# Kernel optimization log

Hardware: AMD Instinct MI355X
Metric: run time of the kernel (lower is better)

## Reference

```python
import jax, jax.numpy as jnp
import numpy as np

# Key observation: the TF module groups ROIs per image (boolean_mask), runs the
# same MLP on each group, concatenates the ragged results, then argsort-gathers
# to restore the ORIGINAL row order. Since the Dense/ReLU MLP acts row-wise and
# identically for every image, the group -> MLP -> regroup pipeline is exactly
# equivalent to applying the MLP to all rows in their original order. The clean
# JAX reference therefore computes the same math with a single fused GEMM chain.

NUM_CLASSES = 81
HIDDEN_DIM = 1024
N = 2048          # total ROIs
SS = 7            # sample_size
FS = 256          # feature_size
FEAT_DIM = SS * SS * FS  # 12544
NUM_IMAGES = 8


def setup_inputs() -> dict:
    key = jax.random.key(0)
    ks = jax.random.split(key, 8)
    features = jax.random.normal(ks[0], (N, SS, SS, FS), dtype=jnp.float32)
    batch_indices = jnp.sort(jax.random.randint(ks[1], (N,), 0, NUM_IMAGES, dtype=jnp.int32))
    s1 = 1.0 / np.sqrt(FEAT_DIM)
    s2 = 1.0 / np.sqrt(HIDDEN_DIM)
    W1 = jax.random.uniform(ks[2], (FEAT_DIM, HIDDEN_DIM), jnp.float32, -s1, s1)
    b1 = jnp.zeros((HIDDEN_DIM,), jnp.float32)
    W2 = jax.random.uniform(ks[3], (HIDDEN_DIM, HIDDEN_DIM), jnp.float32, -s2, s2)
    b2 = jnp.zeros((HIDDEN_DIM,), jnp.float32)
    Wc = jax.random.uniform(ks[4], (HIDDEN_DIM, NUM_CLASSES), jnp.float32, -s2, s2)
    bc = jnp.zeros((NUM_CLASSES,), jnp.float32)
    return {"features": features, "batch_indices": batch_indices,
            "W1": W1, "b1": b1, "W2": W2, "b2": b2, "Wc": Wc, "bc": bc}


def reference(features, batch_indices, W1, b1, W2, b2, Wc, bc):
    # Group/ungroup in the original is an identity permutation on rows, but we
    # reproduce it explicitly and cheaply: stable-sort rows by image id, run the
    # MLP, then invert the permutation via argsort (same as TF argsort-gather).
    order = jnp.argsort(batch_indices, stable=True)          # group rows per image
    x = features[order].reshape(features.shape[0], -1)       # [N, feat_dim]
    x = jax.nn.relu(x @ W1 + b1)
    x = jax.nn.relu(x @ W2 + b2)
    logits = x @ Wc + bc                                     # [N, num_classes]
    inv = jnp.argsort(order)                                 # restore original order
    return logits[inv]
```

## Files before the change

kernel.cpp:

```cpp
#include <hip/hip_runtime.h>
#include <hip/hip_bf16.h>
#include <stdint.h>

typedef __bf16 bf16_t;
typedef __bf16 bf16x2 __attribute__((ext_vector_type(2)));
typedef __bf16 bf16x4 __attribute__((ext_vector_type(4)));
typedef __bf16 bf16x8 __attribute__((ext_vector_type(8)));
typedef float f32x4 __attribute__((ext_vector_type(4)));

__device__ __forceinline__ void async_ld16(const bf16_t* g, bf16_t* lds) {
    __builtin_amdgcn_global_load_lds(
        (__attribute__((address_space(1))) void*)g,
        (__attribute__((address_space(3))) void*)lds,
        16, 0, 0);
}

__device__ __forceinline__ void wait_vm0() {
    asm volatile("s_waitcnt vmcnt(0)" ::: "memory");
}


__device__ __forceinline__ void transpose_tile(
    const float* __restrict__ in, bf16_t* __restrict__ out,
    int R, int C, int Cp, int tileIdx, int tid, float (*tile)[33])
{
    const int tilesX = Cp / 32;
    const int c0 = (tileIdx % tilesX) * 32;
    const int r0 = (tileIdx / tilesX) * 32;
    const int tx = tid & 31;
    const int ty = tid >> 5;
#pragma unroll
    for (int i = 0; i < 32; i += 8) {
        int rr = r0 + ty + i, cc = c0 + tx;
        float v = 0.f;
        if (cc < C) v = in[(size_t)rr * C + cc];
        tile[ty + i][tx] = v;
    }
    __syncthreads();
    const int px = tid & 15;
    const int py = tid >> 4;
#pragma unroll
    for (int i = 0; i < 32; i += 16) {
        int oc = c0 + py + i;
        int orr = r0 + px * 2;
        bf16x2 o = { (bf16_t)tile[px * 2][py + i], (bf16_t)tile[px * 2 + 1][py + i] };
        *(bf16x2*)&out[(size_t)oc * R + orr] = o;
    }
}

__global__ void prep_all(const float* __restrict__ X, bf16_t* __restrict__ Xb, int n4,
                         const float* __restrict__ W1, bf16_t* __restrict__ W1T,
                         const float* __restrict__ W2, bf16_t* __restrict__ W2T,
                         const float* __restrict__ Wc, bf16_t* __restrict__ WcT,
                         int FEAT, int HID, int NC, int NCP,
                         int nCvt, int t1, int t2)
{
    __shared__ float tile[32][33];
    int bid = blockIdx.x;
    int tid = threadIdx.x;
    if (bid < nCvt) {
        int i = bid * 256 + tid;
        if (i < n4) {
            float4 v = ((const float4*)X)[i];
            bf16x4 o = { (bf16_t)v.x, (bf16_t)v.y, (bf16_t)v.z, (bf16_t)v.w };
            ((bf16x4*)Xb)[i] = o;
        }
        return;
    }
    bid -= nCvt;
    if (bid < t1) { transpose_tile(W1, W1T, FEAT, HID, HID, bid, tid, tile); return; }
    bid -= t1;
    if (bid < t2) { transpose_tile(W2, W2T, HID, HID, HID, bid, tid, tile); return; }
    bid -= t2;
    transpose_tile(Wc, WcT, HID, NC, NCP, bid, tid, tile);
}

__global__ __launch_bounds__(256, 2) void gemm128_bk64(
    const bf16_t* __restrict__ A, const bf16_t* __restrict__ B,
    float* __restrict__ P, int M, int N, int K, int KC)
{
    __shared__ __align__(16) bf16_t Asm[2][128 * 64];
    __shared__ __align__(16) bf16_t Bsm[2][128 * 64];

    const int tid  = threadIdx.x;
    const int wave = tid >> 6;
    const int lane = tid & 63;
    const int bm = blockIdx.x, bn = blockIdx.y, s = blockIdx.z;

    const int Koff = s * KC;
    const int Kc   = (K - Koff < KC) ? (K - Koff) : KC;
    const int nt   = Kc >> 6;

    const bf16_t* Ab = A + (size_t)bm * 128 * K + Koff;
    const bf16_t* Bb = B + (size_t)bn * 128 * K + Koff;

    const int sr = lane >> 3;
    const int sk = ((lane & 7) ^ (sr & 7)) * 8;

    const int wm = (wave >> 1) * 64;
    const int wn = (wave & 1) * 64;
    const int r  = lane & 15;
    const int q  = lane >> 4;

    f32x4 acc[4][4];
#pragma unroll
    for (int i = 0; i < 4; ++i)
#pragma unroll
        for (int j = 0; j < 4; ++j)
            acc[i][j] = f32x4{0.f, 0.f, 0.f, 0.f};

    auto issue = [&](int t, int buf) {
#pragma unroll
        for (int i = 0; i < 4; ++i) {
            const int rb = wave * 32 + i * 8;
            async_ld16(Ab + (size_t)(rb + sr) * K + (t * 64 + sk), &Asm[buf][rb * 64]);
            async_ld16(Bb + (size_t)(rb + sr) * K + (t * 64 + sk), &Bsm[buf][rb * 64]);
        }
    };

    issue(0, 0);
    wait_vm0();
    __builtin_amdgcn_s_barrier();

    int cur = 0;
    for (int t = 0; t < nt; ++t) {
        const bool more = (t + 1 < nt);
        if (more) issue(t + 1, cur ^ 1);

#pragma unroll
        for (int rnd = 0; rnd < 2; ++rnd) {
            bf16x8 af[4], bfr[4];
#pragma unroll
            for (int i = 0; i < 4; ++i)
                af[i] = *(const bf16x8*)&Asm[cur][(wm + i * 16 + r) * 64
                                                  + ((rnd * 4 + q) ^ (r & 7)) * 8];
#pragma unroll
            for (int j = 0; j < 4; ++j)
                bfr[j] = *(const bf16x8*)&Bsm[cur][(wn + j * 16 + r) * 64
                                                   + ((rnd * 4 + q) ^ (r & 7)) * 8];
#pragma unroll
            for (int i = 0; i < 4; ++i)
#pragma unroll
                for (int j = 0; j < 4; ++j)
                    acc[i][j] = __builtin_amdgcn_mfma_f32_16x16x32_bf16(af[i], bfr[j], acc[i][j], 0, 0, 0);
        }

        if (more) {
            wait_vm0();
            __builtin_amdgcn_s_barrier();
            cur ^= 1;
        }
    }

    float* Pb = P + ((size_t)s * M + (size_t)bm * 128) * N + (size_t)bn * 128;
    const int r4 = q * 4;
#pragma unroll
    for (int i = 0; i < 4; ++i)
#pragma unroll
        for (int j = 0; j < 4; ++j)
#pragma unroll
            for (int rg = 0; rg < 4; ++rg)
                Pb[(size_t)(wm + i * 16 + r4 + rg) * N + (wn + j * 16 + r)] = acc[i][j][rg];
}

template <bool RELU, typename OutT>
__global__ __launch_bounds__(256, 4) void gemm64_fused(
    const bf16_t* __restrict__ A, const bf16_t* __restrict__ B,
    const float* __restrict__ bias, OutT* __restrict__ out,
    int K, int Nout)
{
    __shared__ __align__(16) bf16_t Asm[2][64 * 64];
    __shared__ __align__(16) bf16_t Bsm[2][64 * 64];

    const int tid  = threadIdx.x;
    const int wave = tid >> 6;
    const int lane = tid & 63;
    const int bm = blockIdx.x, bn = blockIdx.y;

    const bf16_t* Ab = A + (size_t)bm * 64 * K;
    const bf16_t* Bb = B + (size_t)bn * 64 * K;

    const int sr = lane >> 3;
    const int sk = ((lane & 7) ^ (sr & 7)) * 8;

    const int wm = (wave >> 1) * 32;
    const int wn = (wave & 1) * 32;
    const int r  = lane & 15;
    const int q  = lane >> 4;
    const int nt = K >> 6;

    f32x4 acc[2][2];
#pragma unroll
    for (int i = 0; i < 2; ++i)
#pragma unroll
        for (int j = 0; j < 2; ++j)
            acc[i][j] = f32x4{0.f, 0.f, 0.f, 0.f};

    auto issue = [&](int t, int buf) {
#pragma unroll
        for (int i = 0; i < 2; ++i) {
            const int rb = wave * 16 + i * 8;
            async_ld16(Ab + (size_t)(rb + sr) * K + (t * 64 + sk), &Asm[buf][rb * 64]);
            async_ld16(Bb + (size_t)(rb + sr) * K + (t * 64 + sk), &Bsm[buf][rb * 64]);
        }
    };

    issue(0, 0);
    wait_vm0();
    __builtin_amdgcn_s_barrier();

    int cur = 0;
    for (int t = 0; t < nt; ++t) {
        const bool more = (t + 1 < nt);
        if (more) issue(t + 1, cur ^ 1);

#pragma unroll
        for (int rnd = 0; rnd < 2; ++rnd) {
            bf16x8 af[2], bfr[2];
#pragma unroll
            for (int i = 0; i < 2; ++i)
                af[i] = *(const bf16x8*)&Asm[cur][(wm + i * 16 + r) * 64
                                                  + ((rnd * 4 + q) ^ (r & 7)) * 8];
#pragma unroll
            for (int j = 0; j < 2; ++j)
                bfr[j] = *(const bf16x8*)&Bsm[cur][(wn + j * 16 + r) * 64
                                                   + ((rnd * 4 + q) ^ (r & 7)) * 8];
#pragma unroll
            for (int i = 0; i < 2; ++i)
#pragma unroll
                for (int j = 0; j < 2; ++j)
                    acc[i][j] = __builtin_amdgcn_mfma_f32_16x16x32_bf16(af[i], bfr[j], acc[i][j], 0, 0, 0);
        }

        if (more) {
            wait_vm0();
            __builtin_amdgcn_s_barrier();
            cur ^= 1;
        }
    }

    const int r4 = (lane >> 4) * 4;
    const int c  = lane & 15;
#pragma unroll
    for (int i = 0; i < 2; ++i)
#pragma unroll
        for (int j = 0; j < 2; ++j) {
            const int col = bn * 64 + wn + j * 16 + c;
            if (col < Nout) {
                const float bv = bias[col];
#pragma unroll
                for (int rg = 0; rg < 4; ++rg) {
                    const int row = bm * 64 + wm + i * 16 + r4 + rg;
                    float v = acc[i][j][rg] + bv;
                    if (RELU) v = fmaxf(v, 0.f);
                    out[(size_t)row * Nout + col] = (OutT)v;
                }
            }
        }
}


template <int S>
__global__ void reduce_relu_bf16_k(const float* __restrict__ P, const float* __restrict__ bias,
                                   bf16_t* __restrict__ h, int MN, int Nm1) {
    int i4 = (blockIdx.x * 256 + threadIdx.x) * 4;
    if (i4 >= MN) return;
    int n = i4 & Nm1;
    float4 a = *(const float4*)(bias + n);
#pragma unroll
    for (int s = 0; s < S; ++s) {
        float4 p = *(const float4*)(P + (size_t)s * MN + i4);
        a.x += p.x; a.y += p.y; a.z += p.z; a.w += p.w;
    }
    a.x = fmaxf(a.x, 0.f); a.y = fmaxf(a.y, 0.f);
    a.z = fmaxf(a.z, 0.f); a.w = fmaxf(a.w, 0.f);
    bf16x4 o = { (bf16_t)a.x, (bf16_t)a.y, (bf16_t)a.z, (bf16_t)a.w };
    *(bf16x4*)(h + i4) = o;
}


extern "C" void kernel_launch(void* const* d_in, const int* in_sizes, int n_in,
                              void* d_out, int out_size, void* d_ws, size_t ws_size,
                              hipStream_t stream) {
    const float* X  = (const float*)d_in[0];
    const float* W1 = (const float*)d_in[2];
    const float* b1 = (const float*)d_in[3];
    const float* W2 = (const float*)d_in[4];
    const float* b2 = (const float*)d_in[5];
    const float* Wc = (const float*)d_in[6];
    const float* bc = (const float*)d_in[7];
    float* out = (float*)d_out;

    const int M    = in_sizes[1];
    const int FEAT = in_sizes[0] / M;
    const int HID  = in_sizes[3];
    const int NC   = in_sizes[7];
    const int NCP  = 128;

    char* ws = (char*)d_ws;
    size_t off = 0;
    auto alloc = [&](size_t bytes) {
        char* p = ws + off;
        off += (bytes + 255) & ~(size_t)255;
        return p;
    };
    bf16_t* Xb  = (bf16_t*)alloc((size_t)M * FEAT * 2);
    bf16_t* W1T = (bf16_t*)alloc((size_t)FEAT * HID * 2);
    bf16_t* W2T = (bf16_t*)alloc((size_t)HID * HID * 2);
    bf16_t* WcT = (bf16_t*)alloc((size_t)NCP * HID * 2);
    bf16_t* h1  = (bf16_t*)alloc((size_t)M * HID * 2);
    bf16_t* h2  = (bf16_t*)alloc((size_t)M * HID * 2);
    float*  P   = (float*)(ws + off);

    size_t rem  = ws_size > off ? ws_size - off : 0;
    size_t perS = (size_t)M * HID * 4;
    int S1 = (rem >= 4 * perS) ? 4 : (rem >= 2 * perS) ? 2 : 1;
    int KC1 = ((FEAT / S1 + 63) / 64) * 64;

    int n4   = (M * FEAT) / 4;
    int nCvt = (n4 + 255) / 256;
    int t1 = (HID / 32) * (FEAT / 32);
    int t2 = (HID / 32) * (HID / 32);
    int t3 = (NCP / 32) * (HID / 32);
    prep_all<<<nCvt + t1 + t2 + t3, 256, 0, stream>>>(
        X, Xb, n4, W1, W1T, W2, W2T, Wc, WcT, FEAT, HID, NC, NCP, nCvt, t1, t2);

    gemm128_bk64<<<dim3(M / 128, HID / 128, S1), 256, 0, stream>>>(Xb, W1T, P, M, HID, FEAT, KC1);
    switch (S1) {
        case 4: reduce_relu_bf16_k<4><<<(M * HID / 4 + 255) / 256, 256, 0, stream>>>(P, b1, h1, M * HID, HID - 1); break;
        case 2: reduce_relu_bf16_k<2><<<(M * HID / 4 + 255) / 256, 256, 0, stream>>>(P, b1, h1, M * HID, HID - 1); break;
        default: reduce_relu_bf16_k<1><<<(M * HID / 4 + 255) / 256, 256, 0, stream>>>(P, b1, h1, M * HID, HID - 1); break;
    }

    gemm64_fused<true, bf16_t><<<dim3(M / 64, HID / 64), 256, 0, stream>>>(h1, W2T, b2, h2, HID, HID);

    gemm64_fused<false, float><<<dim3(M / 64, NCP / 64), 256, 0, stream>>>(h2, WcT, bc, out, HID, NC);
}
```

Before: 295.8 us.

## Split prep into grid-stride X convert and 4-tile weight transpose; remap GEMM block order

The single prep kernel is split into a grid-stride X-to-bf16 conversion kernel that issues four loads per iteration, and a weight-transpose kernel in which each block handles four 32x32 tiles stacked along rows, cutting the block count. The GEMM block index is also remapped so consecutive blocks walk the N dimension first, which should improve L2 reuse of the A tiles. The aim is to cut launch and tail overhead and raise memory-level parallelism in the bandwidth-bound preprocessing, at the cost of one extra kernel launch and a larger shared-memory tile per block.

After: 319.8 us. +8.1%, slower.

```diff
diff --git a/kernel.cpp b/kernel.cpp
--- a/kernel.cpp
+++ b/kernel.cpp
@@ -19,60 +19,79 @@
     asm volatile("s_waitcnt vmcnt(0)" ::: "memory");
 }
 
-
-__device__ __forceinline__ void transpose_tile(
+__global__ __launch_bounds__(256) void convert_x(
+    const float* __restrict__ X, bf16_t* __restrict__ Xb, int n4)
+{
+    const int stride = gridDim.x * 256;
+    int i = blockIdx.x * 256 + threadIdx.x;
+    const int lim = n4 - 3 * stride;
+    for (; i < lim; i += 4 * stride) {
+        const float4 v0 = ((const float4*)X)[i];
+        const float4 v1 = ((const float4*)X)[i + stride];
+        const float4 v2 = ((const float4*)X)[i + 2 * stride];
+        const float4 v3 = ((const float4*)X)[i + 3 * stride];
+        bf16x4 o0 = { (bf16_t)v0.x, (bf16_t)v0.y, (bf16_t)v0.z, (bf16_t)v0.w };
+        bf16x4 o1 = { (bf16_t)v1.x, (bf16_t)v1.y, (bf16_t)v1.z, (bf16_t)v1.w };
+        bf16x4 o2 = { (bf16_t)v2.x, (bf16_t)v2.y, (bf16_t)v2.z, (bf16_t)v2.w };
+        bf16x4 o3 = { (bf16_t)v3.x, (bf16_t)v3.y, (bf16_t)v3.z, (bf16_t)v3.w };
+        ((bf16x4*)Xb)[i]              = o0;
+        ((bf16x4*)Xb)[i + stride]     = o1;
+        ((bf16x4*)Xb)[i + 2 * stride] = o2;
+        ((bf16x4*)Xb)[i + 3 * stride] = o3;
+    }
+    for (; i < n4; i += stride) {
+        const float4 v = ((const float4*)X)[i];
+        bf16x4 o = { (bf16_t)v.x, (bf16_t)v.y, (bf16_t)v.z, (bf16_t)v.w };
+        ((bf16x4*)Xb)[i] = o;
+    }
+}
+
+__device__ __forceinline__ void transpose_tile4(
     const float* __restrict__ in, bf16_t* __restrict__ out,
-    int R, int C, int Cp, int tileIdx, int tid, float (*tile)[33])
+    int R, int C, int Cp, int tileIdx, int tid, float (*tile)[32][33])
 {
     const int tilesX = Cp / 32;
     const int c0 = (tileIdx % tilesX) * 32;
-    const int r0 = (tileIdx / tilesX) * 32;
+    const int r0 = (tileIdx / tilesX) * 128;
     const int tx = tid & 31;
     const int ty = tid >> 5;
 #pragma unroll
-    for (int i = 0; i < 32; i += 8) {
-        int rr = r0 + ty + i, cc = c0 + tx;
-        float v = 0.f;
-        if (cc < C) v = in[(size_t)rr * C + cc];
-        tile[ty + i][tx] = v;
-    }
+    for (int s = 0; s < 4; ++s)
+#pragma unroll
+        for (int i = 0; i < 32; i += 8) {
+            int rr = r0 + s * 32 + ty + i, cc = c0 + tx;
+            float v = 0.f;
+            if (cc < C) v = in[(size_t)rr * C + cc];
+            tile[s][ty + i][tx] = v;
+        }
     __syncthreads();
     const int px = tid & 15;
     const int py = tid >> 4;
 #pragma unroll
-    for (int i = 0; i < 32; i += 16) {
-        int oc = c0 + py + i;
-        int orr = r0 + px * 2;
-        bf16x2 o = { (bf16_t)tile[px * 2][py + i], (bf16_t)tile[px * 2 + 1][py + i] };
-        *(bf16x2*)&out[(size_t)oc * R + orr] = o;
-    }
-}
-
-__global__ void prep_all(const float* __restrict__ X, bf16_t* __restrict__ Xb, int n4,
-                         const float* __restrict__ W1, bf16_t* __restrict__ W1T,
-                         const float* __restrict__ W2, bf16_t* __restrict__ W2T,
-                         const float* __restrict__ Wc, bf16_t* __restrict__ WcT,
-                         int FEAT, int HID, int NC, int NCP,
-                         int nCvt, int t1, int t2)
-{
-    __shared__ float tile[32][33];
+    for (int s = 0; s < 4; ++s)
+#pragma unroll
+        for (int i = 0; i < 32; i += 16) {
+            int oc = c0 + py + i;
+            int orr = r0 + s * 32 + px * 2;
+            bf16x2 o = { (bf16_t)tile[s][px * 2][py + i],
+                         (bf16_t)tile[s][px * 2 + 1][py + i] };
+            *(bf16x2*)&out[(size_t)oc * R + orr] = o;
+        }
+}
+
+__global__ void prep_w(const float* __restrict__ W1, bf16_t* __restrict__ W1T,
+                       const float* __restrict__ W2, bf16_t* __restrict__ W2T,
+                       const float* __restrict__ Wc, bf16_t* __restrict__ WcT,
+                       int FEAT, int HID, int NC, int NCP, int t1, int t2)
+{
+    __shared__ float tile[4][32][33];
     int bid = blockIdx.x;
     int tid = threadIdx.x;
-    if (bid < nCvt) {
-        int i = bid * 256 + tid;
-        if (i < n4) {
-            float4 v = ((const float4*)X)[i];
-            bf16x4 o = { (bf16_t)v.x, (bf16_t)v.y, (bf16_t)v.z, (bf16_t)v.w };
-            ((bf16x4*)Xb)[i] = o;
-        }
-        return;
-    }
-    bid -= nCvt;
-    if (bid < t1) { transpose_tile(W1, W1T, FEAT, HID, HID, bid, tid, tile); return; }
+    if (bid < t1) { transpose_tile4(W1, W1T, FEAT, HID, HID, bid, tid, tile); return; }
     bid -= t1;
-    if (bid < t2) { transpose_tile(W2, W2T, HID, HID, HID, bid, tid, tile); return; }
+    if (bid < t2) { transpose_tile4(W2, W2T, HID, HID, HID, bid, tid, tile); return; }
     bid -= t2;
-    transpose_tile(Wc, WcT, HID, NC, NCP, bid, tid, tile);
+    transpose_tile4(Wc, WcT, HID, NC, NCP, bid, tid, tile);
 }
 
 __global__ __launch_bounds__(256, 2) void gemm128_bk64(
@@ -85,7 +104,12 @@
     const int tid  = threadIdx.x;
     const int wave = tid >> 6;
     const int lane = tid & 63;
-    const int bm = blockIdx.x, bn = blockIdx.y, s = blockIdx.z;
+
+    const int o   = blockIdx.x + gridDim.x * (blockIdx.y + gridDim.y * blockIdx.z);
+    const int bn  = o % gridDim.y;
+    const int tmp = o / gridDim.y;
+    const int bm  = tmp % gridDim.x;
+    const int s   = tmp / gridDim.x;
 
     const int Koff = s * KC;
     const int Kc   = (K - Koff < KC) ? (K - Koff) : KC;
@@ -317,13 +341,14 @@
     int S1 = (rem >= 4 * perS) ? 4 : (rem >= 2 * perS) ? 2 : 1;
     int KC1 = ((FEAT / S1 + 63) / 64) * 64;
 
-    int n4   = (M * FEAT) / 4;
-    int nCvt = (n4 + 255) / 256;
-    int t1 = (HID / 32) * (FEAT / 32);
-    int t2 = (HID / 32) * (HID / 32);
-    int t3 = (NCP / 32) * (HID / 32);
-    prep_all<<<nCvt + t1 + t2 + t3, 256, 0, stream>>>(
-        X, Xb, n4, W1, W1T, W2, W2T, Wc, WcT, FEAT, HID, NC, NCP, nCvt, t1, t2);
+    int n4 = (M * FEAT) / 4;
+    convert_x<<<2048, 256, 0, stream>>>(X, Xb, n4);
+
+    int t1 = (FEAT / 128) * (HID / 32);
+    int t2 = (HID / 128) * (HID / 32);
+    int t3 = (HID / 128) * (NCP / 32);
+    prep_w<<<t1 + t2 + t3, 256, 0, stream>>>(
+        W1, W1T, W2, W2T, Wc, WcT, FEAT, HID, NC, NCP, t1, t2);
 
     gemm128_bk64<<<dim3(M / 128, HID / 128, S1), 256, 0, stream>>>(Xb, W1T, P, M, HID, FEAT, KC1);
     switch (S1) {
```
